# Performance work log

Measured on AMD Instinct MI355X. Metric: run time of the kernel, lower is better.

Reference implementation:

```python
import jax, jax.numpy as jnp
import numpy as np
import math

B, H, S, D = 2, 16, 2048, 64

def setup_inputs() -> dict:
    key = jax.random.key(0)
    kq, kk, kv = jax.random.split(key, 3)
    return {
        "q": jax.random.normal(kq, (B, H, S, D), dtype=jnp.float32),
        "k": jax.random.normal(kk, (B, H, S, D), dtype=jnp.float32),
        "v": jax.random.normal(kv, (B, H, S, D), dtype=jnp.float32),
        "temp": jnp.ones((1,), dtype=jnp.float32),
    }

def reference(q, k, v, temp):
    dk = q.shape[-1]
    # scores: [B,H,S,S] = q @ k^T / (temp * sqrt(dk))
    scores = jnp.einsum("bhsd,bhtd->bhst", q, k) / (temp[0] * math.sqrt(dk))
    attention = jax.nn.softmax(scores, axis=-1)
    y = jnp.einsum("bhst,bhtd->bhsd", attention, v)
    return y
```

## Files before the change

### kernel.cpp

```cpp
#include <hip/hip_runtime.h>


typedef _Float16 f16;
typedef __attribute__((ext_vector_type(8))) _Float16 f16x8;
typedef __attribute__((ext_vector_type(4))) _Float16 f16x4;
typedef __attribute__((ext_vector_type(4))) float f32x4;

constexpr int Bc = 2, Hc = 16, Sc = 2048, Dc = 64;
constexpr int BM = 64;
constexpr int BN = 64;
constexpr int LDP = 72;

__global__ __launch_bounds__(256, 4)
void fa3(const float* __restrict__ qp, const float* __restrict__ kp,
         const float* __restrict__ vp, const float* __restrict__ temp,
         float* __restrict__ out) {
  __shared__ f16 Pbuf[BM * LDP];
  __shared__ float Lred[4][BM];

  const int tid = threadIdx.x, lane = tid & 63, w = tid >> 6;
  const int lq = lane & 15, qd = lane >> 4;
  const int L = blockIdx.x;
  const int bh = L & 31;
  const int qt = L >> 5;

  const float scale = 1.0f / (temp[0] * 8.0f);
  const size_t base = (size_t)bh * Sc * Dc;
  const float* qg = qp + base + (size_t)qt * BM * Dc;
  const float* kg = kp + base;
  const float* vg = vp + base;

  f16x8 Qf[4][2];
#pragma unroll
  for (int nt = 0; nt < 4; ++nt)
#pragma unroll
    for (int kc = 0; kc < 2; ++kc) {
      const float* p = qg + (16 * nt + lq) * Dc + 32 * kc + 8 * qd;
      f32x4 a = *(const f32x4*)p;
      f32x4 b = *(const f32x4*)(p + 4);
      Qf[nt][kc] = (f16x8){(f16)a.x, (f16)a.y, (f16)a.z, (f16)a.w,
                           (f16)b.x, (f16)b.y, (f16)b.z, (f16)b.w};
    }

  f32x4 Oa[4];
  float ls[4];
#pragma unroll
  for (int i = 0; i < 4; ++i) { Oa[i] = (f32x4){0.f, 0.f, 0.f, 0.f}; ls[i] = 0.f; }

  for (int kt = 0; kt < Sc / BN; ++kt) {
    const float* kb = kg + ((size_t)kt * BN + 16 * w + lq) * Dc;
    f16x8 Kf[2];
#pragma unroll
    for (int kc = 0; kc < 2; ++kc) {
      f32x4 a = *(const f32x4*)(kb + 32 * kc + 8 * qd);
      f32x4 b = *(const f32x4*)(kb + 32 * kc + 8 * qd + 4);
      Kf[kc] = (f16x8){(f16)a.x, (f16)a.y, (f16)a.z, (f16)a.w,
                       (f16)b.x, (f16)b.y, (f16)b.z, (f16)b.w};
    }

    const float* vb = vg + (size_t)kt * BN * Dc + 16 * w + lq;
    f16x8 Vf[2];
#pragma unroll
    for (int kc = 0; kc < 2; ++kc) {
      float t0 = vb[(32 * kc + 8 * qd + 0) * Dc];
      float t1 = vb[(32 * kc + 8 * qd + 1) * Dc];
      float t2 = vb[(32 * kc + 8 * qd + 2) * Dc];
      float t3 = vb[(32 * kc + 8 * qd + 3) * Dc];
      float t4 = vb[(32 * kc + 8 * qd + 4) * Dc];
      float t5 = vb[(32 * kc + 8 * qd + 5) * Dc];
      float t6 = vb[(32 * kc + 8 * qd + 6) * Dc];
      float t7 = vb[(32 * kc + 8 * qd + 7) * Dc];
      Vf[kc] = (f16x8){(f16)t0, (f16)t1, (f16)t2, (f16)t3,
                       (f16)t4, (f16)t5, (f16)t6, (f16)t7};
    }

    f32x4 St[4];
#pragma unroll
    for (int nt = 0; nt < 4; ++nt) {
      f32x4 acc = (f32x4){0.f, 0.f, 0.f, 0.f};
      acc = __builtin_amdgcn_mfma_f32_16x16x32_f16(Kf[0], Qf[nt][0], acc, 0, 0, 0);
      acc = __builtin_amdgcn_mfma_f32_16x16x32_f16(Kf[1], Qf[nt][1], acc, 0, 0, 0);
      St[nt] = acc;
    }

    __syncthreads();

#pragma unroll
    for (int nt = 0; nt < 4; ++nt) {
      float p0 = __expf(St[nt].x * scale);
      float p1 = __expf(St[nt].y * scale);
      float p2 = __expf(St[nt].z * scale);
      float p3 = __expf(St[nt].w * scale);
      ls[nt] += (p0 + p1) + (p2 + p3);
      *(f16x4*)&Pbuf[(16 * nt + lq) * LDP + 16 * w + 4 * qd] =
          (f16x4){(f16)p0, (f16)p1, (f16)p2, (f16)p3};
    }

    __syncthreads();

#pragma unroll
    for (int mt = 0; mt < 4; ++mt) {
      f16x8 P0 = *(const f16x8*)&Pbuf[(16 * mt + lq) * LDP + 8 * qd];
      f16x8 P1 = *(const f16x8*)&Pbuf[(16 * mt + lq) * LDP + 32 + 8 * qd];
      f32x4 acc = Oa[mt];
      acc = __builtin_amdgcn_mfma_f32_16x16x32_f16(P0, Vf[0], acc, 0, 0, 0);
      acc = __builtin_amdgcn_mfma_f32_16x16x32_f16(P1, Vf[1], acc, 0, 0, 0);
      Oa[mt] = acc;
    }
  }

#pragma unroll
  for (int nt = 0; nt < 4; ++nt) {
    float l = ls[nt];
    l += __shfl_xor(l, 16, 64);
    l += __shfl_xor(l, 32, 64);
    ls[nt] = l;
  }
  if (qd == 0) {
#pragma unroll
    for (int nt = 0; nt < 4; ++nt) Lred[w][16 * nt + lq] = ls[nt];
  }
  __syncthreads();

  float* og = out + base + (size_t)qt * BM * Dc + 16 * w + lq;
#pragma unroll
  for (int mt = 0; mt < 4; ++mt)
#pragma unroll
    for (int r = 0; r < 4; ++r) {
      int row = 16 * mt + 4 * qd + r;
      float l = Lred[0][row] + Lred[1][row] + Lred[2][row] + Lred[3][row];
      og[(size_t)row * Dc] = Oa[mt][r] / l;
    }
}

extern "C" void kernel_launch(void* const* d_in, const int* in_sizes, int n_in,
                              void* d_out, int out_size, void* d_ws, size_t ws_size,
                              hipStream_t stream) {
  const float* q    = (const float*)d_in[0];
  const float* k    = (const float*)d_in[1];
  const float* v    = (const float*)d_in[2];
  const float* temp = (const float*)d_in[3];
  float* out = (float*)d_out;

  dim3 grid(Bc * Hc * (Sc / BM));
  dim3 block(256);
  fa3<<<grid, block, 0, stream>>>(q, k, v, temp, out);
}
```

Before: 169.7 us.

## Pre-convert K/V to fp16 with transposed V and drop LDS P round-trip

New measurement: 188.7 us. 1.11x slower.

```diff
diff --git a/kernel.cpp b/kernel.cpp
--- a/kernel.cpp
+++ b/kernel.cpp
@@ -7,16 +7,50 @@
 typedef __attribute__((ext_vector_type(4))) float f32x4;
 
 constexpr int Bc = 2, Hc = 16, Sc = 2048, Dc = 64;
-constexpr int BM = 64;
-constexpr int BN = 64;
-constexpr int LDP = 72;
+constexpr size_t NE = (size_t)Bc * Hc * Sc * Dc;
 
-__global__ __launch_bounds__(256, 4)
-void fa3(const float* __restrict__ qp, const float* __restrict__ kp,
-         const float* __restrict__ vp, const float* __restrict__ temp,
-         float* __restrict__ out) {
-  __shared__ f16 Pbuf[BM * LDP];
-  __shared__ float Lred[4][BM];
+__global__ __launch_bounds__(256)
+void prep(const float* __restrict__ kp, const float* __restrict__ vp,
+          const float* __restrict__ temp,
+          f16* __restrict__ kh, f16* __restrict__ vt) {
+  __shared__ f16 T[64][68];
+  const int tid = threadIdx.x;
+  const int bh = blockIdx.x & 31;
+  const int st = blockIdx.x >> 5;
+  const float ksc = 1.44269504088896340736f / (temp[0] * 8.0f);
+
+  const size_t base = (size_t)bh * Sc * Dc + (size_t)st * 64 * Dc;
+  const float* kg = kp + base;
+  const float* vg = vp + base;
+  f16* khg = kh + base;
+
+#pragma unroll
+  for (int i = 0; i < 4; ++i) {
+    int f = tid + (i << 8);
+    f32x4 a = *(const f32x4*)(kg + f * 4);
+    *(f16x4*)(khg + f * 4) = (f16x4){(f16)(a.x * ksc), (f16)(a.y * ksc),
+                                     (f16)(a.z * ksc), (f16)(a.w * ksc)};
+    f32x4 b = *(const f32x4*)(vg + f * 4);
+    int r = f >> 4, c = (f & 15) << 2;
+    T[c + 0][r] = (f16)b.x; T[c + 1][r] = (f16)b.y;
+    T[c + 2][r] = (f16)b.z; T[c + 3][r] = (f16)b.w;
+  }
+  __syncthreads();
+  f16* vtg = vt + (size_t)bh * Dc * Sc + st * 64;
+#pragma unroll
+  for (int i = 0; i < 4; ++i) {
+    int f = tid + (i << 8);
+    int d = f >> 4, c4 = (f & 15) << 2;
+    *(f16x4*)(vtg + (size_t)d * Sc + c4) = *(const f16x4*)&T[d][c4];
+  }
+}
+
+__global__ __launch_bounds__(256, 2)
+void fa4(const float* __restrict__ qp, const f16* __restrict__ kh,
+         const f16* __restrict__ vt, float* __restrict__ out) {
+  __shared__ float OsA[64][66];
+  __shared__ float OsB[64][66];
+  __shared__ float Lred[4][64];
 
   const int tid = threadIdx.x, lane = tid & 63, w = tid >> 6;
   const int lq = lane & 15, qd = lane >> 4;
@@ -24,11 +58,10 @@
   const int bh = L & 31;
   const int qt = L >> 5;
 
-  const float scale = 1.0f / (temp[0] * 8.0f);
   const size_t base = (size_t)bh * Sc * Dc;
-  const float* qg = qp + base + (size_t)qt * BM * Dc;
-  const float* kg = kp + base;
-  const float* vg = vp + base;
+  const float* qg = qp + base + (size_t)qt * 64 * Dc;
+  const f16* kg = kh + base;
+  const f16* vg = vt + (size_t)bh * Dc * Sc;
 
   f16x8 Qf[4][2];
 #pragma unroll
@@ -42,71 +75,67 @@
                            (f16)b.x, (f16)b.y, (f16)b.z, (f16)b.w};
     }
 
-  f32x4 Oa[4];
+  f32x4 Oa[4][4];
   float ls[4];
 #pragma unroll
-  for (int i = 0; i < 4; ++i) { Oa[i] = (f32x4){0.f, 0.f, 0.f, 0.f}; ls[i] = 0.f; }
+  for (int nt = 0; nt < 4; ++nt) {
+    ls[nt] = 0.f;
+#pragma unroll
+    for (int dt = 0; dt < 4; ++dt) Oa[nt][dt] = (f32x4){0.f, 0.f, 0.f, 0.f};
+  }
 
-  for (int kt = 0; kt < Sc / BN; ++kt) {
-    const float* kb = kg + ((size_t)kt * BN + 16 * w + lq) * Dc;
-    f16x8 Kf[2];
+  auto loadK = [&](int kt, f16x8& k0, f16x8& k1) {
+    const f16* kb = kg + ((size_t)(kt * 64 + 16 * w + lq)) * Dc;
+    k0 = *(const f16x8*)(kb + 8 * qd);
+    k1 = *(const f16x8*)(kb + 32 + 8 * qd);
+  };
+  auto loadV = [&](int kt, f16x4* vf) {
+    const f16* vb = vg + kt * 64 + 16 * w + 4 * qd;
 #pragma unroll
-    for (int kc = 0; kc < 2; ++kc) {
-      f32x4 a = *(const f32x4*)(kb + 32 * kc + 8 * qd);
-      f32x4 b = *(const f32x4*)(kb + 32 * kc + 8 * qd + 4);
-      Kf[kc] = (f16x8){(f16)a.x, (f16)a.y, (f16)a.z, (f16)a.w,
-                       (f16)b.x, (f16)b.y, (f16)b.z, (f16)b.w};
-    }
+    for (int dt = 0; dt < 4; ++dt)
+      vf[dt] = *(const f16x4*)(vb + (size_t)(16 * dt + lq) * Sc);
+  };
 
-    const float* vb = vg + (size_t)kt * BN * Dc + 16 * w + lq;
-    f16x8 Vf[2];
-#pragma unroll
-    for (int kc = 0; kc < 2; ++kc) {
-      float t0 = vb[(32 * kc + 8 * qd + 0) * Dc];
-      float t1 = vb[(32 * kc + 8 * qd + 1) * Dc];
-      float t2 = vb[(32 * kc + 8 * qd + 2) * Dc];
-      float t3 = vb[(32 * kc + 8 * qd + 3) * Dc];
-      float t4 = vb[(32 * kc + 8 * qd + 4) * Dc];
-      float t5 = vb[(32 * kc + 8 * qd + 5) * Dc];
-      float t6 = vb[(32 * kc + 8 * qd + 6) * Dc];
-      float t7 = vb[(32 * kc + 8 * qd + 7) * Dc];
-      Vf[kc] = (f16x8){(f16)t0, (f16)t1, (f16)t2, (f16)t3,
-                       (f16)t4, (f16)t5, (f16)t6, (f16)t7};
-    }
+  f16x8 Kc0, Kc1, Kn0, Kn1;
+  f16x4 Vc[4], Vn[4];
+  loadK(0, Kc0, Kc1);
+  loadV(0, Vc);
+
+  for (int kt = 0; kt < Sc / 64; ++kt) {
+    int ktn = kt + 1 < Sc / 64 ? kt + 1 : kt;
+    loadK(ktn, Kn0, Kn1);
+    loadV(ktn, Vn);
 
     f32x4 St[4];
 #pragma unroll
     for (int nt = 0; nt < 4; ++nt) {
       f32x4 acc = (f32x4){0.f, 0.f, 0.f, 0.f};
-      acc = __builtin_amdgcn_mfma_f32_16x16x32_f16(Kf[0], Qf[nt][0], acc, 0, 0, 0);
-      acc = __builtin_amdgcn_mfma_f32_16x16x32_f16(Kf[1], Qf[nt][1], acc, 0, 0, 0);
+      acc = __builtin_amdgcn_mfma_f32_16x16x32_f16(Kc0, Qf[nt][0], acc, 0, 0, 0);
+      acc = __builtin_amdgcn_mfma_f32_16x16x32_f16(Kc1, Qf[nt][1], acc, 0, 0, 0);
       St[nt] = acc;
     }
 
-    __syncthreads();
+    f16x4 Pf[4];
+#pragma unroll
+    for (int nt = 0; nt < 4; ++nt) {
+      float p0 = exp2f(St[nt].x);
+      float p1 = exp2f(St[nt].y);
+      float p2 = exp2f(St[nt].z);
+      float p3 = exp2f(St[nt].w);
+      ls[nt] += (p0 + p1) + (p2 + p3);
+      Pf[nt] = (f16x4){(f16)p0, (f16)p1, (f16)p2, (f16)p3};
+    }
 
 #pragma unroll
-    for (int nt = 0; nt < 4; ++nt) {
-      float p0 = __expf(St[nt].x * scale);
-      float p1 = __expf(St[nt].y * scale);
-      float p2 = __expf(St[nt].z * scale);
-      float p3 = __expf(St[nt].w * scale);
-      ls[nt] += (p0 + p1) + (p2 + p3);
-      *(f16x4*)&Pbuf[(16 * nt + lq) * LDP + 16 * w + 4 * qd] =
-          (f16x4){(f16)p0, (f16)p1, (f16)p2, (f16)p3};
-    }
+    for (int nt = 0; nt < 4; ++nt)
+#pragma unroll
+      for (int dt = 0; dt < 4; ++dt)
+        Oa[nt][dt] =
+            __builtin_amdgcn_mfma_f32_16x16x16f16(Pf[nt], Vc[dt], Oa[nt][dt], 0, 0, 0);
 
-    __syncthreads();
-
+    Kc0 = Kn0; Kc1 = Kn1;
 #pragma unroll
-    for (int mt = 0; mt < 4; ++mt) {
-      f16x8 P0 = *(const f16x8*)&Pbuf[(16 * mt + lq) * LDP + 8 * qd];
-      f16x8 P1 = *(const f16x8*)&Pbuf[(16 * mt + lq) * LDP + 32 + 8 * qd];
-      f32x4 acc = Oa[mt];
-      acc = __builtin_amdgcn_mfma_f32_16x16x32_f16(P0, Vf[0], acc, 0, 0, 0);
-      acc = __builtin_amdgcn_mfma_f32_16x16x32_f16(P1, Vf[1], acc, 0, 0, 0);
-      Oa[mt] = acc;
-    }
+    for (int dt = 0; dt < 4; ++dt) Vc[dt] = Vn[dt];
   }
 
 #pragma unroll
@@ -114,23 +143,39 @@
     float l = ls[nt];
     l += __shfl_xor(l, 16, 64);
     l += __shfl_xor(l, 32, 64);
-    ls[nt] = l;
+    if (qd == 0) Lred[w][16 * nt + lq] = l;
   }
-  if (qd == 0) {
+
+  float(&Os)[64][66] = (w & 2) ? OsB : OsA;
+  if (!(w & 1)) {
 #pragma unroll
-    for (int nt = 0; nt < 4; ++nt) Lred[w][16 * nt + lq] = ls[nt];
+    for (int nt = 0; nt < 4; ++nt)
+#pragma unroll
+      for (int dt = 0; dt < 4; ++dt)
+#pragma unroll
+        for (int r = 0; r < 4; ++r)
+          Os[16 * nt + 4 * qd + r][16 * dt + lq] = Oa[nt][dt][r];
+  }
+  __syncthreads();
+  if (w & 1) {
+#pragma unroll
+    for (int nt = 0; nt < 4; ++nt)
+#pragma unroll
+      for (int dt = 0; dt < 4; ++dt)
+#pragma unroll
+        for (int r = 0; r < 4; ++r)
+          Os[16 * nt + 4 * qd + r][16 * dt + lq] += Oa[nt][dt][r];
   }
   __syncthreads();
 
-  float* og = out + base + (size_t)qt * BM * Dc + 16 * w + lq;
+  float* og = out + base + (size_t)qt * 64 * Dc;
 #pragma unroll
-  for (int mt = 0; mt < 4; ++mt)
-#pragma unroll
-    for (int r = 0; r < 4; ++r) {
-      int row = 16 * mt + 4 * qd + r;
-      float l = Lred[0][row] + Lred[1][row] + Lred[2][row] + Lred[3][row];
-      og[(size_t)row * Dc] = Oa[mt][r] / l;
-    }
+  for (int r = 0; r < 16; ++r) {
+    int row = 16 * w + r;
+    float l = Lred[0][row] + Lred[1][row] + Lred[2][row] + Lred[3][row];
+    float vo = OsA[row][lane] + OsB[row][lane];
+    og[(size_t)row * Dc + lane] = vo / l;
+  }
 }
 
 extern "C" void kernel_launch(void* const* d_in, const int* in_sizes, int n_in,
@@ -142,7 +187,10 @@
   const float* temp = (const float*)d_in[3];
   float* out = (float*)d_out;
 
-  dim3 grid(Bc * Hc * (Sc / BM));
+  f16* kh = (f16*)d_ws;
+  f16* vt = kh + NE;
+
   dim3 block(256);
-  fa3<<<grid, block, 0, stream>>>(q, k, v, temp, out);
+  prep<<<dim3(Bc * Hc * (Sc / 64)), block, 0, stream>>>(k, v, temp, kh, vt);
+  fa4<<<dim3(Bc * Hc * (Sc / 64)), block, 0, stream>>>(q, kh, vt, out);
 }
```
